# Kernel tuning notes

Hardware: AMD Instinct MI355X
Metric: run time of the kernel (lower is better)

Reference implementation:

```python
import jax, jax.numpy as jnp
import numpy as np

N = 1024        # total atoms
H = 256         # hidden_dim
L = 512         # latent_dim
NG = 50         # n_gaussians
NI = 3          # n_interactions
CUTOFF = 5.0
MAXZ = 100
B = 16          # molecules (N // 64 atoms each)

CENTERS = jnp.linspace(0.0, CUTOFF, NG)
WIDTH = 0.5 * (CUTOFF / NG)   # scalar, same for all gaussians
LN_EPS = 1e-5

def gelu(x):
    return jax.nn.gelu(x, approximate=False)  # torch default GELU is exact erf

def setup_inputs() -> dict:
    key = jax.random.key(0)
    ks = jax.random.split(key, 24)
    s = 0.05
    inp = {
        'z': jax.random.randint(ks[0], (N,), 0, MAXZ),
        'pos': jax.random.uniform(ks[1], (N, 3), dtype=jnp.float32) * 10.0,  # 10 A box
        'batch': jnp.arange(N, dtype=jnp.int32) // (N // B),
        'emb': jax.random.normal(ks[2], (MAXZ, H), dtype=jnp.float32),
        # per-interaction params stacked over layer axis (NI)
        'fw1': jax.random.normal(ks[3], (NI, NG, H), dtype=jnp.float32) * s,
        'fb1': jnp.zeros((NI, H), jnp.float32),
        'fw2': jax.random.normal(ks[4], (NI, H, H), dtype=jnp.float32) * s,
        'fb2': jnp.zeros((NI, H), jnp.float32),
        'aw1': jax.random.normal(ks[5], (NI, H, H), dtype=jnp.float32) * s,
        'ab1': jnp.zeros((NI, H), jnp.float32),
        'aw2': jax.random.normal(ks[6], (NI, H, H), dtype=jnp.float32) * s,
        'ab2': jnp.zeros((NI, H), jnp.float32),
        # projection head
        'pw1': jax.random.normal(ks[7], (H, H), dtype=jnp.float32) * s,
        'pb1': jnp.zeros((H,), jnp.float32),
        'pw2': jax.random.normal(ks[8], (H, L), dtype=jnp.float32) * s,
        'pb2': jnp.zeros((L,), jnp.float32),
        'ln_g': jnp.ones((L,), jnp.float32),
        'ln_b': jnp.zeros((L,), jnp.float32),
    }
    return inp

def _interaction(h, pos, fw1, fb1, fw2, fb2, aw1, ab1, aw2, ab2):
    diff = pos[None, :, :] - pos[:, None, :]              # [N,N,3]
    dist = jnp.linalg.norm(diff, axis=-1)                  # [N,N]
    mask = (dist < CUTOFF) & (dist > 1e-6)                 # [N,N]
    rbf = jnp.exp(-((dist[..., None] - CENTERS) ** 2) / (2.0 * WIDTH ** 2))  # [N,N,NG]
    W = gelu(rbf @ fw1 + fb1) @ fw2 + fb2                  # [N,N,H] filter MLP
    Wm = W * mask[..., None].astype(W.dtype)
    # agg[i,c] = sum_j Wm[i,j,c] * h[j,c]
    agg = jnp.einsum('ijc,jc->ic', Wm, h)
    return gelu(agg @ aw1 + ab1) @ aw2 + ab2

def reference(z, pos, batch, emb, fw1, fb1, fw2, fb2, aw1, ab1, aw2, ab2,
              pw1, pb1, pw2, pb2, ln_g, ln_b):
    h = emb[z]                                             # [N,H]
    for i in range(NI):
        h = h + _interaction(h, pos, fw1[i], fb1[i], fw2[i], fb2[i],
                             aw1[i], ab1[i], aw2[i], ab2[i])
    pooled = jax.ops.segment_sum(h, batch, num_segments=B)  # [B,H]
    x = gelu(pooled @ pw1 + pb1) @ pw2 + pb2               # [B,L]
    mu = jnp.mean(x, axis=-1, keepdims=True)
    var = jnp.var(x, axis=-1, keepdims=True)
    return (x - mu) / jnp.sqrt(var + LN_EPS) * ln_g + ln_b
```

## Files before the change

### kernel.cpp

```cpp
#include <hip/hip_runtime.h>
#include <hip/hip_fp16.h>
#include <math.h>

#define N 1024
#define H 256
#define L 512
#define NG 50
#define NI 3
#define B 16
#define NBINS 2048
#define CUT 5.0f
#define BPB 16
#define TROWS (NBINS + 1)
#define MATB 4
#define CAP 768
#define APAD 264

typedef __attribute__((ext_vector_type(8))) short bf16x8;
typedef __attribute__((ext_vector_type(4))) float f32x4;

#define FMA4(A_, S_, V_) do { \
    (A_).x = fmaf((S_), (V_).x, (A_).x); (A_).y = fmaf((S_), (V_).y, (A_).y); \
    (A_).z = fmaf((S_), (V_).z, (A_).z); (A_).w = fmaf((S_), (V_).w, (A_).w); } while (0)

__device__ __forceinline__ float gelu_f(float x) {
    return 0.5f * x * (1.0f + erff(x * 0.70710678118654752f));
}
__device__ __forceinline__ unsigned short f2bf(float f) {
    unsigned u = __float_as_uint(f);
    unsigned r = (u + 0x7fffu + ((u >> 16) & 1u)) >> 16;
    return (unsigned short)r;
}

__global__ void __launch_bounds__(256) setup_k(
        const int* __restrict__ z, const float* __restrict__ emb,
        const float* __restrict__ pos, float* __restrict__ h,
        __half* __restrict__ hhf, int* __restrict__ meta,
        int* __restrict__ cnts, const float* __restrict__ fw2,
        unsigned short* __restrict__ Bt, __half* __restrict__ Wtb) {
    int tid = threadIdx.x;
    if (blockIdx.x >= N) {
        int blk = blockIdx.x - N;
        int l = blk / H, ch = blk % H;
        float v = fw2[((size_t)l * H + tid) * H + ch];
        Bt[((size_t)l * H + ch) * H + tid] = f2bf(v);
        if (tid == 0)
            Wtb[((size_t)l * TROWS + NBINS) * H + ch] = __float2half(0.f);
        return;
    }
    int i = blockIdx.x;
    float v = emb[z[i] * H + tid];
    h[i * H + tid] = v;
    hhf[i * H + tid] = __float2half(v);

    __shared__ int sCnt;
    __shared__ int sMeta[CAP];
    if (tid == 0) sCnt = 0;
    __syncthreads();
    float pix = pos[i * 3 + 0], piy = pos[i * 3 + 1], piz = pos[i * 3 + 2];
    const float invd = (float)NBINS / CUT;
    for (int r = 0; r < 4; ++r) {
        int j = tid + r * 256;
        float dx = pos[j * 3 + 0] - pix;
        float dy = pos[j * 3 + 1] - piy;
        float dz = pos[j * 3 + 2] - piz;
        float d = sqrtf(dx * dx + dy * dy + dz * dz);
        if (d < CUT && d > 1e-6f) {
            int bin = (int)(d * invd);
            if (bin > NBINS - 1) bin = NBINS - 1;
            int idx = atomicAdd(&sCnt, 1);
            sMeta[idx] = j | (bin << 10);
        }
    }
    __syncthreads();
    int cnt = sCnt;
    int pc = (cnt + 31) & ~31;
    for (int t = cnt + tid; t < pc; t += 256)
        sMeta[t] = i | (NBINS << 10);
    __syncthreads();
    for (int t = tid; t < pc; t += 256)
        meta[(size_t)i * CAP + t] = sMeta[t];
    if (tid == 0) cnts[i] = pc;
}

__global__ void __launch_bounds__(256) table_k(
        const float* __restrict__ fw1, const float* __restrict__ fb1,
        const unsigned short* __restrict__ Bt, const float* __restrict__ fb2,
        __half* __restrict__ Wtb) {
    const int bpl = NBINS / BPB;
    int layer = blockIdx.x / bpl;
    int blk = blockIdx.x % bpl;
    int b0 = blk * BPB;
    int tid = threadIdx.x;
    int wid = tid >> 6, lane = tid & 63;
    int c4 = lane * 4;
    int ub = wid * 4;
    const float* lfw1 = fw1 + layer * NG * H;
    __half* lWt = Wtb + (size_t)layer * TROWS * H;

    __shared__ __align__(16) float sW1[NG][H];
    __shared__ __align__(16) float sRbf[BPB][56];
    __shared__ __align__(16) unsigned short sAb[BPB][APAD];
    const float delta = CUT / (float)NBINS;
    for (int idx = tid; idx < NG * (H / 4); idx += 256) {
        int k = idx >> 6;
        int c = (idx & 63) * 4;
        *(float4*)&sW1[k][c] = *(const float4*)(lfw1 + k * H + c);
    }
    for (int idx = tid; idx < BPB * NG; idx += 256) {
        int u = idx & 15;
        int k = idx >> 4;
        float d = ((float)(b0 + u) + 0.5f) * delta;
        float t = d - (float)k * (CUT / 49.0f);
        sRbf[u][k] = expf(t * t * -200.0f);
    }
    __syncthreads();

    float4 acc1[4];
    #pragma unroll
    for (int u = 0; u < 4; ++u) acc1[u] = make_float4(0.f, 0.f, 0.f, 0.f);
    for (int kq = 0; kq < 12; ++kq) {
        int k = kq * 4;
        float4 r0 = *(const float4*)&sRbf[ub + 0][k];
        float4 r1 = *(const float4*)&sRbf[ub + 1][k];
        float4 r2 = *(const float4*)&sRbf[ub + 2][k];
        float4 r3 = *(const float4*)&sRbf[ub + 3][k];
        float4 q0 = *(const float4*)&sW1[k + 0][c4];
        float4 q1 = *(const float4*)&sW1[k + 1][c4];
        float4 q2 = *(const float4*)&sW1[k + 2][c4];
        float4 q3 = *(const float4*)&sW1[k + 3][c4];
        FMA4(acc1[0], r0.x, q0); FMA4(acc1[0], r0.y, q1);
        FMA4(acc1[0], r0.z, q2); FMA4(acc1[0], r0.w, q3);
        FMA4(acc1[1], r1.x, q0); FMA4(acc1[1], r1.y, q1);
        FMA4(acc1[1], r1.z, q2); FMA4(acc1[1], r1.w, q3);
        FMA4(acc1[2], r2.x, q0); FMA4(acc1[2], r2.y, q1);
        FMA4(acc1[2], r2.z, q2); FMA4(acc1[2], r2.w, q3);
        FMA4(acc1[3], r3.x, q0); FMA4(acc1[3], r3.y, q1);
        FMA4(acc1[3], r3.z, q2); FMA4(acc1[3], r3.w, q3);
    }
    for (int k = 48; k < NG; ++k) {
        float4 q = *(const float4*)&sW1[k][c4];
        #pragma unroll
        for (int u = 0; u < 4; ++u) FMA4(acc1[u], sRbf[ub + u][k], q);
    }
    float4 b1 = *(const float4*)(fb1 + layer * H + c4);
    #pragma unroll
    for (int u = 0; u < 4; ++u) {
        ushort4 g;
        g.x = f2bf(gelu_f(acc1[u].x + b1.x));
        g.y = f2bf(gelu_f(acc1[u].y + b1.y));
        g.z = f2bf(gelu_f(acc1[u].z + b1.z));
        g.w = f2bf(gelu_f(acc1[u].w + b1.w));
        *(ushort4*)&sAb[ub + u][c4] = g;
    }
    __syncthreads();

    int m = lane & 15;
    int quad = lane >> 4;
    bf16x8 afr[8];
    #pragma unroll
    for (int c = 0; c < 8; ++c)
        afr[c] = *(const bf16x8*)&sAb[m][c * 32 + quad * 8];
    #pragma unroll
    for (int ct = 0; ct < 4; ++ct) {
        int chn = (wid * 4 + ct) * 16 + m;
        const bf16x8* Bv = (const bf16x8*)(Bt + ((size_t)layer * H + chn) * H);
        f32x4 acc = {0.f, 0.f, 0.f, 0.f};
        #pragma unroll
        for (int c = 0; c < 8; ++c)
            acc = __builtin_amdgcn_mfma_f32_16x16x32_bf16(afr[c], Bv[c * 4 + quad],
                                                          acc, 0, 0, 0);
        float bias = fb2[layer * H + chn];
        #pragma unroll
        for (int r = 0; r < 4; ++r) {
            int bin = b0 + quad * 4 + r;
            lWt[(size_t)bin * H + chn] = __float2half(acc[r] + bias);
        }
    }
}

__global__ void __launch_bounds__(256) pair_k(
    const __half* __restrict__ hhf, const __half* __restrict__ Wt,
    const int* __restrict__ gmeta, const int* __restrict__ cnts,
    float* __restrict__ aggP) {
    int tid = threadIdx.x;
    int wid = tid >> 6, lane = tid & 63;
    int c4 = lane * 4;
    int i = blockIdx.x >> 1;
    int half = blockIdx.x & 1;
    int stream = half * 4 + wid;

    __shared__ int sMeta[CAP];
    __shared__ __align__(16) float sPart[4][H];

    int pc = cnts[i];
    for (int t = tid; t < pc; t += 256)
        sMeta[t] = gmeta[(size_t)i * CAP + t];
    __syncthreads();

    float4 acc = make_float4(0.f, 0.f, 0.f, 0.f);
    int groups = pc >> 5;

    uint2 wA[4], wB[4];
    uint2 hA[4], hB[4];

    auto issue = [&](int g, uint2 (&wr)[4], uint2 (&hr)[4]) {
        #pragma unroll
        for (int s = 0; s < 4; ++s) {
            int n = stream + (g * 4 + s) * 8;
            int p = sMeta[n];
            int j = p & 1023;
            int bin = p >> 10;
            wr[s] = *(const uint2*)(Wt + (size_t)bin * H + c4);
            hr[s] = *(const uint2*)(hhf + (size_t)j * H + c4);
        }
    };
    auto consume = [&](uint2 (&wr)[4], uint2 (&hr)[4]) {
        #pragma unroll
        for (int s = 0; s < 4; ++s) {
            __half2 w01 = *(__half2*)&wr[s].x;
            __half2 w23 = *(__half2*)&wr[s].y;
            __half2 h01 = *(__half2*)&hr[s].x;
            __half2 h23 = *(__half2*)&hr[s].y;
            acc.x += __half2float(w01.x) * __half2float(h01.x);
            acc.y += __half2float(w01.y) * __half2float(h01.y);
            acc.z += __half2float(w23.x) * __half2float(h23.x);
            acc.w += __half2float(w23.y) * __half2float(h23.y);
        }
    };

    if (groups > 0) {
        issue(0, wA, hA);
        if (groups > 1) issue(1, wB, hB);
        for (int g = 0; g < groups; g += 2) {
            consume(wA, hA);
            if (g + 2 < groups) issue(g + 2, wA, hA);
            if (g + 1 < groups) {
                consume(wB, hB);
                if (g + 3 < groups) issue(g + 3, wB, hB);
            }
        }
    }
    *(float4*)&sPart[wid][c4] = acc;
    __syncthreads();
    aggP[((size_t)half * N + i) * H + tid] =
        sPart[0][tid] + sPart[1][tid] + sPart[2][tid] + sPart[3][tid];
}

__global__ void __launch_bounds__(512) mlp_k(
    const float* __restrict__ aggP, const float* __restrict__ hin,
    const float* __restrict__ aw1, const float* __restrict__ ab1,
    const float* __restrict__ aw2, const float* __restrict__ ab2,
    float* __restrict__ hout, __half* __restrict__ hhf_out) {
    int tid = threadIdx.x;
    int wid = tid >> 6, lane = tid & 63;
    int c4 = lane * 4;
    int i0 = blockIdx.x * MATB;
    __shared__ __align__(16) float sAT[H][MATB];
    __shared__ __align__(16) float sGT[H][MATB];
    __shared__ __align__(16) float sPart[8][MATB][H];

    if (tid < H) {
        #pragma unroll
        for (int r = 0; r < MATB; ++r)
            sAT[tid][r] = aggP[(size_t)(i0 + r) * H + tid]
                        + aggP[((size_t)N + i0 + r) * H + tid];
    }
    __syncthreads();

    int k0 = wid * 32;
    float4 acc[MATB];
    #pragma unroll
    for (int a = 0; a < MATB; ++a) acc[a] = make_float4(0.f, 0.f, 0.f, 0.f);
    #pragma unroll 8
    for (int k = 0; k < 32; ++k) {
        float4 q = *(const float4*)(aw1 + (k0 + k) * H + c4);
        float4 act = *(const float4*)&sAT[k0 + k][0];
        FMA4(acc[0], act.x, q); FMA4(acc[1], act.y, q);
        FMA4(acc[2], act.z, q); FMA4(acc[3], act.w, q);
    }
    #pragma unroll
    for (int a = 0; a < MATB; ++a)
        *(float4*)&sPart[wid][a][c4] = acc[a];
    __syncthreads();
    if (tid < H) {
        float b1 = ab1[tid];
        float g[MATB];
        #pragma unroll
        for (int a = 0; a < MATB; ++a) {
            float v = b1;
            #pragma unroll
            for (int s = 0; s < 8; ++s) v += sPart[s][a][tid];
            g[a] = gelu_f(v);
        }
        *(float4*)&sGT[tid][0] = make_float4(g[0], g[1], g[2], g[3]);
    }
    __syncthreads();
    #pragma unroll
    for (int a = 0; a < MATB; ++a) acc[a] = make_float4(0.f, 0.f, 0.f, 0.f);
    #pragma unroll 8
    for (int k = 0; k < 32; ++k) {
        float4 q = *(const float4*)(aw2 + (k0 + k) * H + c4);
        float4 act = *(const float4*)&sGT[k0 + k][0];
        FMA4(acc[0], act.x, q); FMA4(acc[1], act.y, q);
        FMA4(acc[2], act.z, q); FMA4(acc[3], act.w, q);
    }
    #pragma unroll
    for (int a = 0; a < MATB; ++a)
        *(float4*)&sPart[wid][a][c4] = acc[a];
    __syncthreads();
    if (tid < H) {
        float b2 = ab2[tid];
        #pragma unroll
        for (int a = 0; a < MATB; ++a) {
            float v = b2;
            #pragma unroll
            for (int s = 0; s < 8; ++s) v += sPart[s][a][tid];
            float hv = hin[(i0 + a) * H + tid] + v;
            hout[(i0 + a) * H + tid] = hv;
            hhf_out[(i0 + a) * H + tid] = __float2half(hv);
        }
    }
}

__global__ void __launch_bounds__(256) head_k(
        const float* __restrict__ h,
        const float* __restrict__ pw1, const float* __restrict__ pb1,
        const float* __restrict__ pw2, const float* __restrict__ pb2,
        const float* __restrict__ ln_g, const float* __restrict__ ln_b,
        float* __restrict__ out) {
    int b = blockIdx.x, tid = threadIdx.x;
    int wid = tid >> 6, lane = tid & 63;
    int c4 = lane * 4;
    __shared__ float sP[H];
    __shared__ __align__(16) float sPw[4][H];
    __shared__ float sG[H];
    __shared__ __align__(16) float sP2[4][L];
    __shared__ float sX[L];
    __shared__ float sRed[256];

    float4 p = make_float4(0.f, 0.f, 0.f, 0.f);
    #pragma unroll 4
    for (int a = 0; a < 16; ++a) {
        float4 hv = *(const float4*)(h + (b * 64 + wid * 16 + a) * H + c4);
        p.x += hv.x; p.y += hv.y; p.z += hv.z; p.w += hv.w;
    }
    *(float4*)&sPw[wid][c4] = p;
    __syncthreads();
    sP[tid] = sPw[0][tid] + sPw[1][tid] + sPw[2][tid] + sPw[3][tid];
    __syncthreads();

    int k0 = wid * 64;
    float4 acc = make_float4(0.f, 0.f, 0.f, 0.f);
    #pragma unroll 8
    for (int k = 0; k < 64; ++k) {
        float4 q = *(const float4*)(pw1 + (k0 + k) * H + c4);
        float s = sP[k0 + k];
        FMA4(acc, s, q);
    }
    *(float4*)&sPw[wid][c4] = acc;
    __syncthreads();
    sG[tid] = gelu_f(pb1[tid] + sPw[0][tid] + sPw[1][tid] + sPw[2][tid] + sPw[3][tid]);
    __syncthreads();

    float4 a0 = make_float4(0.f, 0.f, 0.f, 0.f);
    float4 a1 = make_float4(0.f, 0.f, 0.f, 0.f);
    #pragma unroll 4
    for (int k = 0; k < 64; ++k) {
        float s = sG[k0 + k];
        float4 q0 = *(const float4*)(pw2 + (k0 + k) * L + lane * 8);
        float4 q1 = *(const float4*)(pw2 + (k0 + k) * L + lane * 8 + 4);
        FMA4(a0, s, q0);
        FMA4(a1, s, q1);
    }
    *(float4*)&sP2[wid][lane * 8] = a0;
    *(float4*)&sP2[wid][lane * 8 + 4] = a1;
    __syncthreads();
    for (int r = 0; r < 2; ++r) {
        int l = tid + r * 256;
        sX[l] = pb2[l] + sP2[0][l] + sP2[1][l] + sP2[2][l] + sP2[3][l];
    }
    __syncthreads();

    sRed[tid] = sX[tid] + sX[tid + 256];
    __syncthreads();
    for (int off = 128; off > 0; off >>= 1) {
        if (tid < off) sRed[tid] += sRed[tid + off];
        __syncthreads();
    }
    float mu = sRed[0] / (float)L;
    __syncthreads();
    float d0 = sX[tid] - mu, d1 = sX[tid + 256] - mu;
    sRed[tid] = d0 * d0 + d1 * d1;
    __syncthreads();
    for (int off = 128; off > 0; off >>= 1) {
        if (tid < off) sRed[tid] += sRed[tid + off];
        __syncthreads();
    }
    float var = sRed[0] / (float)L;
    float rstd = rsqrtf(var + 1e-5f);
    for (int r = 0; r < 2; ++r) {
        int l = tid + r * 256;
        out[b * L + l] = (sX[l] - mu) * rstd * ln_g[l] + ln_b[l];
    }
}

extern "C" void kernel_launch(void* const* d_in, const int* in_sizes, int n_in,
                              void* d_out, int out_size, void* d_ws, size_t ws_size,
                              hipStream_t stream) {
    const int*   z    = (const int*)d_in[0];
    const float* pos  = (const float*)d_in[1];
    const float* emb  = (const float*)d_in[3];
    const float* fw1  = (const float*)d_in[4];
    const float* fb1  = (const float*)d_in[5];
    const float* fw2  = (const float*)d_in[6];
    const float* fb2  = (const float*)d_in[7];
    const float* aw1  = (const float*)d_in[8];
    const float* ab1  = (const float*)d_in[9];
    const float* aw2  = (const float*)d_in[10];
    const float* ab2  = (const float*)d_in[11];
    const float* pw1  = (const float*)d_in[12];
    const float* pb1  = (const float*)d_in[13];
    const float* pw2  = (const float*)d_in[14];
    const float* pb2  = (const float*)d_in[15];
    const float* ln_g = (const float*)d_in[16];
    const float* ln_b = (const float*)d_in[17];
    float* out = (float*)d_out;

    float* hA  = (float*)d_ws;
    float* hB  = hA + N * H;
    float* aggP = hB + N * H;
    __half* hhfA = (__half*)(aggP + 2 * N * H);
    __half* hhfB = hhfA + N * H;
    __half* Wtb  = hhfB + N * H;
    int* meta = (int*)(Wtb + (size_t)NI * TROWS * H);
    int* cnts = meta + (size_t)N * CAP;
    unsigned short* Bt = (unsigned short*)(cnts + N);

    setup_k<<<N + NI * H, 256, 0, stream>>>(z, emb, pos, hA, hhfA, meta, cnts,
                                            fw2, Bt, Wtb);
    table_k<<<NI * (NBINS / BPB), 256, 0, stream>>>(fw1, fb1, Bt, fb2, Wtb);
    float* hin = hA;  __half* hbin = hhfA;
    float* hout = hB; __half* hbout = hhfB;
    for (int it = 0; it < NI; ++it) {
        pair_k<<<2 * N, 256, 0, stream>>>(hbin, Wtb + (size_t)it * TROWS * H,
                                          meta, cnts, aggP);
        mlp_k<<<N / MATB, 512, 0, stream>>>(aggP, hin, aw1 + it * H * H, ab1 + it * H,
                                            aw2 + it * H * H, ab2 + it * H, hout, hbout);
        float* t1 = hin; hin = hout; hout = t1;
        __half* t2 = hbin; hbin = hbout; hbout = t2;
    }
    head_k<<<B, 256, 0, stream>>>(hin, pw1, pb1, pw2, pb2, ln_g, ln_b, out);
}
```

Measured before the change: 238.1 us.

## Fuse pair aggregation with atom MLP and use wave-ballot neighbor compaction

Merges the pair aggregation kernel and the per-atom MLP kernel into one kernel that handles two atoms per 512-thread block. Each atom's neighbor list is split over four waves, and the partial sums are reduced in shared memory straight into the MLP input. This removes the global aggP round trip and one launch per layer. Setup now compacts neighbors with a per-wave ballot and a single atomic instead of one atomic per pair. The trade-off is that aw1/aw2 are reread for only two atoms per block instead of four, and the block is larger with more shared memory.

```diff
diff --git a/kernel.cpp b/kernel.cpp
--- a/kernel.cpp
+++ b/kernel.cpp
@@ -12,7 +12,7 @@
 #define CUT 5.0f
 #define BPB 16
 #define TROWS (NBINS + 1)
-#define MATB 4
+#define FA 2
 #define CAP 768
 #define APAD 264
 
@@ -59,17 +59,23 @@
     __syncthreads();
     float pix = pos[i * 3 + 0], piy = pos[i * 3 + 1], piz = pos[i * 3 + 2];
     const float invd = (float)NBINS / CUT;
+    int lane = tid & 63;
     for (int r = 0; r < 4; ++r) {
         int j = tid + r * 256;
         float dx = pos[j * 3 + 0] - pix;
         float dy = pos[j * 3 + 1] - piy;
         float dz = pos[j * 3 + 2] - piz;
         float d = sqrtf(dx * dx + dy * dy + dz * dz);
-        if (d < CUT && d > 1e-6f) {
+        bool keep = (d < CUT && d > 1e-6f);
+        unsigned long long mk = __ballot(keep);
+        int base = 0;
+        if (lane == 0) base = atomicAdd(&sCnt, (int)__popcll(mk));
+        base = __shfl(base, 0);
+        if (keep) {
             int bin = (int)(d * invd);
             if (bin > NBINS - 1) bin = NBINS - 1;
-            int idx = atomicAdd(&sCnt, 1);
-            sMeta[idx] = j | (bin << 10);
+            int off = (int)__popcll(mk & ((1ull << lane) - 1ull));
+            sMeta[base + off] = j | (bin << 10);
         }
     }
     __syncthreads();
@@ -179,49 +185,60 @@
     }
 }
 
-__global__ void __launch_bounds__(256) pair_k(
+__global__ void __launch_bounds__(512) pm_k(
     const __half* __restrict__ hhf, const __half* __restrict__ Wt,
     const int* __restrict__ gmeta, const int* __restrict__ cnts,
-    float* __restrict__ aggP) {
+    const float* __restrict__ hin,
+    const float* __restrict__ aw1, const float* __restrict__ ab1,
+    const float* __restrict__ aw2, const float* __restrict__ ab2,
+    float* __restrict__ hout, __half* __restrict__ hhf_out) {
     int tid = threadIdx.x;
     int wid = tid >> 6, lane = tid & 63;
     int c4 = lane * 4;
-    int i = blockIdx.x >> 1;
-    int half = blockIdx.x & 1;
-    int stream = half * 4 + wid;
-
-    __shared__ int sMeta[CAP];
-    __shared__ __align__(16) float sPart[4][H];
-
-    int pc = cnts[i];
-    for (int t = tid; t < pc; t += 256)
-        sMeta[t] = gmeta[(size_t)i * CAP + t];
-    __syncthreads();
-
+    int i0 = blockIdx.x * FA;
+    int a = wid >> 2;
+    int st = wid & 3;
+
+    __shared__ int sMeta[FA][CAP];
+    __shared__ __align__(16) float sPP[4][FA][H];
+    __shared__ __align__(16) float sAT[H][FA];
+    __shared__ __align__(16) float sGT[H][FA];
+    __shared__ __align__(16) float sPart[8][FA][H];
+
+    {
+        int aa = tid >> 8;
+        int t0 = tid & 255;
+        int pcs = cnts[i0 + aa];
+        for (int t = t0; t < pcs; t += 256)
+            sMeta[aa][t] = gmeta[(size_t)(i0 + aa) * CAP + t];
+    }
+    __syncthreads();
+
+    int pc = cnts[i0 + a];
     float4 acc = make_float4(0.f, 0.f, 0.f, 0.f);
-    int groups = pc >> 5;
+    int groups = pc >> 4;
 
     uint2 wA[4], wB[4];
     uint2 hA[4], hB[4];
 
     auto issue = [&](int g, uint2 (&wr)[4], uint2 (&hr)[4]) {
         #pragma unroll
-        for (int s = 0; s < 4; ++s) {
-            int n = stream + (g * 4 + s) * 8;
-            int p = sMeta[n];
+        for (int u = 0; u < 4; ++u) {
+            int n = st + (g * 4 + u) * 4;
+            int p = sMeta[a][n];
             int j = p & 1023;
             int bin = p >> 10;
-            wr[s] = *(const uint2*)(Wt + (size_t)bin * H + c4);
-            hr[s] = *(const uint2*)(hhf + (size_t)j * H + c4);
+            wr[u] = *(const uint2*)(Wt + (size_t)bin * H + c4);
+            hr[u] = *(const uint2*)(hhf + (size_t)j * H + c4);
         }
     };
     auto consume = [&](uint2 (&wr)[4], uint2 (&hr)[4]) {
         #pragma unroll
-        for (int s = 0; s < 4; ++s) {
-            __half2 w01 = *(__half2*)&wr[s].x;
-            __half2 w23 = *(__half2*)&wr[s].y;
-            __half2 h01 = *(__half2*)&hr[s].x;
-            __half2 h23 = *(__half2*)&hr[s].y;
+        for (int u = 0; u < 4; ++u) {
+            __half2 w01 = *(__half2*)&wr[u].x;
+            __half2 w23 = *(__half2*)&wr[u].y;
+            __half2 h01 = *(__half2*)&hr[u].x;
+            __half2 h23 = *(__half2*)&hr[u].y;
             acc.x += __half2float(w01.x) * __half2float(h01.x);
             acc.y += __half2float(w01.y) * __half2float(h01.y);
             acc.z += __half2float(w23.x) * __half2float(h23.x);
@@ -241,85 +258,55 @@
             }
         }
     }
-    *(float4*)&sPart[wid][c4] = acc;
-    __syncthreads();
-    aggP[((size_t)half * N + i) * H + tid] =
-        sPart[0][tid] + sPart[1][tid] + sPart[2][tid] + sPart[3][tid];
-}
-
-__global__ void __launch_bounds__(512) mlp_k(
-    const float* __restrict__ aggP, const float* __restrict__ hin,
-    const float* __restrict__ aw1, const float* __restrict__ ab1,
-    const float* __restrict__ aw2, const float* __restrict__ ab2,
-    float* __restrict__ hout, __half* __restrict__ hhf_out) {
-    int tid = threadIdx.x;
-    int wid = tid >> 6, lane = tid & 63;
-    int c4 = lane * 4;
-    int i0 = blockIdx.x * MATB;
-    __shared__ __align__(16) float sAT[H][MATB];
-    __shared__ __align__(16) float sGT[H][MATB];
-    __shared__ __align__(16) float sPart[8][MATB][H];
-
-    if (tid < H) {
-        #pragma unroll
-        for (int r = 0; r < MATB; ++r)
-            sAT[tid][r] = aggP[(size_t)(i0 + r) * H + tid]
-                        + aggP[((size_t)N + i0 + r) * H + tid];
+    *(float4*)&sPP[st][a][c4] = acc;
+    __syncthreads();
+    {
+        int aa = tid >> 8, ch = tid & 255;
+        sAT[ch][aa] = sPP[0][aa][ch] + sPP[1][aa][ch]
+                    + sPP[2][aa][ch] + sPP[3][aa][ch];
     }
     __syncthreads();
 
     int k0 = wid * 32;
-    float4 acc[MATB];
-    #pragma unroll
-    for (int a = 0; a < MATB; ++a) acc[a] = make_float4(0.f, 0.f, 0.f, 0.f);
+    float4 m0 = make_float4(0.f, 0.f, 0.f, 0.f);
+    float4 m1 = make_float4(0.f, 0.f, 0.f, 0.f);
     #pragma unroll 8
     for (int k = 0; k < 32; ++k) {
         float4 q = *(const float4*)(aw1 + (k0 + k) * H + c4);
-        float4 act = *(const float4*)&sAT[k0 + k][0];
-        FMA4(acc[0], act.x, q); FMA4(acc[1], act.y, q);
-        FMA4(acc[2], act.z, q); FMA4(acc[3], act.w, q);
-    }
-    #pragma unroll
-    for (int a = 0; a < MATB; ++a)
-        *(float4*)&sPart[wid][a][c4] = acc[a];
-    __syncthreads();
-    if (tid < H) {
-        float b1 = ab1[tid];
-        float g[MATB];
-        #pragma unroll
-        for (int a = 0; a < MATB; ++a) {
-            float v = b1;
-            #pragma unroll
-            for (int s = 0; s < 8; ++s) v += sPart[s][a][tid];
-            g[a] = gelu_f(v);
-        }
-        *(float4*)&sGT[tid][0] = make_float4(g[0], g[1], g[2], g[3]);
-    }
-    __syncthreads();
-    #pragma unroll
-    for (int a = 0; a < MATB; ++a) acc[a] = make_float4(0.f, 0.f, 0.f, 0.f);
+        float2 act = *(const float2*)&sAT[k0 + k][0];
+        FMA4(m0, act.x, q); FMA4(m1, act.y, q);
+    }
+    *(float4*)&sPart[wid][0][c4] = m0;
+    *(float4*)&sPart[wid][1][c4] = m1;
+    __syncthreads();
+    {
+        int aa = tid >> 8, ch = tid & 255;
+        float v = ab1[ch];
+        #pragma unroll
+        for (int w2 = 0; w2 < 8; ++w2) v += sPart[w2][aa][ch];
+        sGT[ch][aa] = gelu_f(v);
+    }
+    __syncthreads();
+
+    m0 = make_float4(0.f, 0.f, 0.f, 0.f);
+    m1 = make_float4(0.f, 0.f, 0.f, 0.f);
     #pragma unroll 8
     for (int k = 0; k < 32; ++k) {
         float4 q = *(const float4*)(aw2 + (k0 + k) * H + c4);
-        float4 act = *(const float4*)&sGT[k0 + k][0];
-        FMA4(acc[0], act.x, q); FMA4(acc[1], act.y, q);
-        FMA4(acc[2], act.z, q); FMA4(acc[3], act.w, q);
-    }
-    #pragma unroll
-    for (int a = 0; a < MATB; ++a)
-        *(float4*)&sPart[wid][a][c4] = acc[a];
-    __syncthreads();
-    if (tid < H) {
-        float b2 = ab2[tid];
-        #pragma unroll
-        for (int a = 0; a < MATB; ++a) {
-            float v = b2;
-            #pragma unroll
-            for (int s = 0; s < 8; ++s) v += sPart[s][a][tid];
-            float hv = hin[(i0 + a) * H + tid] + v;
-            hout[(i0 + a) * H + tid] = hv;
-            hhf_out[(i0 + a) * H + tid] = __float2half(hv);
-        }
+        float2 act = *(const float2*)&sGT[k0 + k][0];
+        FMA4(m0, act.x, q); FMA4(m1, act.y, q);
+    }
+    *(float4*)&sPart[wid][0][c4] = m0;
+    *(float4*)&sPart[wid][1][c4] = m1;
+    __syncthreads();
+    {
+        int aa = tid >> 8, ch = tid & 255;
+        float v = ab2[ch];
+        #pragma unroll
+        for (int w2 = 0; w2 < 8; ++w2) v += sPart[w2][aa][ch];
+        float hv = hin[(size_t)(i0 + aa) * H + ch] + v;
+        hout[(size_t)(i0 + aa) * H + ch] = hv;
+        hhf_out[(size_t)(i0 + aa) * H + ch] = __float2half(hv);
     }
 }
 
@@ -443,10 +430,11 @@
     float* hin = hA;  __half* hbin = hhfA;
     float* hout = hB; __half* hbout = hhfB;
     for (int it = 0; it < NI; ++it) {
-        pair_k<<<2 * N, 256, 0, stream>>>(hbin, Wtb + (size_t)it * TROWS * H,
-                                          meta, cnts, aggP);
-        mlp_k<<<N / MATB, 512, 0, stream>>>(aggP, hin, aw1 + it * H * H, ab1 + it * H,
-                                            aw2 + it * H * H, ab2 + it * H, hout, hbout);
+        pm_k<<<N / FA, 512, 0, stream>>>(hbin, Wtb + (size_t)it * TROWS * H,
+                                         meta, cnts, hin,
+                                         aw1 + it * H * H, ab1 + it * H,
+                                         aw2 + it * H * H, ab2 + it * H,
+                                         hout, hbout);
         float* t1 = hin; hin = hout; hout = t1;
         __half* t2 = hbin; hbin = hbout; hbout = t2;
     }
```

Result: no change. 242.6 us (+1.9%).

## Use wave-aggregated atomics for neighbor lists and read pair metadata directly from global memory

Applied to the files above, without the earlier changes.

Neighbor-list building now does one shared atomicAdd per wavefront, using a ballot and popcount prefix, instead of one per kept pair. In pair_k the shared-memory staging of metadata and its barrier are removed. Each wave instead reads a contiguous slice of the metadata from global memory as int4, makes it wave-uniform with readfirstlane, and computes addresses with shifts. The metadata loads are software-pipelined ahead of the gather loads. The slice-per-stream partition relies on the padded count being a multiple of 32, and it changes the neighbor ordering and summation order.

```diff
diff --git a/kernel.cpp b/kernel.cpp
--- a/kernel.cpp
+++ b/kernel.cpp
@@ -59,17 +59,23 @@
     __syncthreads();
     float pix = pos[i * 3 + 0], piy = pos[i * 3 + 1], piz = pos[i * 3 + 2];
     const float invd = (float)NBINS / CUT;
+    int lane = tid & 63;
     for (int r = 0; r < 4; ++r) {
         int j = tid + r * 256;
         float dx = pos[j * 3 + 0] - pix;
         float dy = pos[j * 3 + 1] - piy;
         float dz = pos[j * 3 + 2] - piz;
         float d = sqrtf(dx * dx + dy * dy + dz * dz);
-        if (d < CUT && d > 1e-6f) {
+        bool keep = (d < CUT && d > 1e-6f);
+        unsigned long long mk = __ballot(keep);
+        int base = 0;
+        if (lane == 0) base = atomicAdd(&sCnt, (int)__popcll(mk));
+        base = __shfl(base, 0);
+        if (keep) {
             int bin = (int)(d * invd);
             if (bin > NBINS - 1) bin = NBINS - 1;
-            int idx = atomicAdd(&sCnt, 1);
-            sMeta[idx] = j | (bin << 10);
+            int off = (int)__popcll(mk & ((1ull << lane) - 1ull));
+            sMeta[base + off] = j | (bin << 10);
         }
     }
     __syncthreads();
@@ -190,38 +196,42 @@
     int half = blockIdx.x & 1;
     int stream = half * 4 + wid;
 
-    __shared__ int sMeta[CAP];
     __shared__ __align__(16) float sPart[4][H];
 
     int pc = cnts[i];
-    for (int t = tid; t < pc; t += 256)
-        sMeta[t] = gmeta[(size_t)i * CAP + t];
-    __syncthreads();
+    int len = pc >> 3;
+    int chunks = len >> 2;
+    int sbase = __builtin_amdgcn_readfirstlane(stream * len);
+    const int* mptr = gmeta + (size_t)i * CAP + sbase;
+    const char* WtB = (const char*)Wt;
+    const char* hhB = (const char*)hhf;
+    int choffB = lane * 8;
 
     float4 acc = make_float4(0.f, 0.f, 0.f, 0.f);
-    int groups = pc >> 5;
-
-    uint2 wA[4], wB[4];
-    uint2 hA[4], hB[4];
-
-    auto issue = [&](int g, uint2 (&wr)[4], uint2 (&hr)[4]) {
-        #pragma unroll
-        for (int s = 0; s < 4; ++s) {
-            int n = stream + (g * 4 + s) * 8;
-            int p = sMeta[n];
-            int j = p & 1023;
-            int bin = p >> 10;
-            wr[s] = *(const uint2*)(Wt + (size_t)bin * H + c4);
-            hr[s] = *(const uint2*)(hhf + (size_t)j * H + c4);
-        }
+    int4 mA, mB;
+    uint2 wA[4], hA[4], wB[4], hB[4];
+
+    auto ldmeta = [&](int c) -> int4 {
+        return *(const int4*)(mptr + c * 4);
+    };
+    auto one = [&](int p, uint2& wr, uint2& hr) {
+        p = __builtin_amdgcn_readfirstlane(p);
+        int j = p & 1023;
+        int bin = p >> 10;
+        wr = *(const uint2*)(WtB + (((unsigned)bin << 9) | (unsigned)choffB));
+        hr = *(const uint2*)(hhB + (((unsigned)j << 9) | (unsigned)choffB));
+    };
+    auto issueD = [&](const int4& m, uint2 (&wr)[4], uint2 (&hr)[4]) {
+        one(m.x, wr[0], hr[0]); one(m.y, wr[1], hr[1]);
+        one(m.z, wr[2], hr[2]); one(m.w, wr[3], hr[3]);
     };
     auto consume = [&](uint2 (&wr)[4], uint2 (&hr)[4]) {
         #pragma unroll
-        for (int s = 0; s < 4; ++s) {
-            __half2 w01 = *(__half2*)&wr[s].x;
-            __half2 w23 = *(__half2*)&wr[s].y;
-            __half2 h01 = *(__half2*)&hr[s].x;
-            __half2 h23 = *(__half2*)&hr[s].y;
+        for (int u = 0; u < 4; ++u) {
+            __half2 w01 = *(__half2*)&wr[u].x;
+            __half2 w23 = *(__half2*)&wr[u].y;
+            __half2 h01 = *(__half2*)&hr[u].x;
+            __half2 h23 = *(__half2*)&hr[u].y;
             acc.x += __half2float(w01.x) * __half2float(h01.x);
             acc.y += __half2float(w01.y) * __half2float(h01.y);
             acc.z += __half2float(w23.x) * __half2float(h23.x);
@@ -229,16 +239,17 @@
         }
     };
 
-    if (groups > 0) {
-        issue(0, wA, hA);
-        if (groups > 1) issue(1, wB, hB);
-        for (int g = 0; g < groups; g += 2) {
+    if (chunks > 0) {
+        mA = ldmeta(0);
+        if (chunks > 1) mB = ldmeta(1);
+        issueD(mA, wA, hA);
+        for (int c = 0; c < chunks; c += 2) {
+            if (c + 2 < chunks) mA = ldmeta(c + 2);
+            if (c + 1 < chunks) issueD(mB, wB, hB);
             consume(wA, hA);
-            if (g + 2 < groups) issue(g + 2, wA, hA);
-            if (g + 1 < groups) {
-                consume(wB, hB);
-                if (g + 3 < groups) issue(g + 3, wB, hB);
-            }
+            if (c + 3 < chunks) mB = ldmeta(c + 3);
+            if (c + 2 < chunks) issueD(mA, wA, hA);
+            if (c + 1 < chunks) consume(wB, hB);
         }
     }
     *(float4*)&sPart[wid][c4] = acc;
```

New measurement: 233.1 us. 1.02x faster.
